# Optimization experiments

Measured on AMD Instinct MI355X. Metric: run time of the kernel, lower is better.

## Reference

```python
import jax, jax.numpy as jnp
import numpy as np

B, C, H, W = 8, 384, 32, 32
NUM_HEADS = 8
HEAD_DIM = C // NUM_HEADS


def setup_inputs() -> dict:
    key = jax.random.key(0)
    k1, k2, k3, k4, k5 = jax.random.split(key, 5)
    s = 1.0 / np.sqrt(C)
    return {
        "x": jax.random.normal(k1, (B, C, H, W), dtype=jnp.float32),
        "w_qkv": jax.random.normal(k2, (3 * C, C), dtype=jnp.float32) * s,   # 1x1 conv == linear over channels
        "b_qkv": jax.random.normal(k3, (3 * C,), dtype=jnp.float32) * 0.01,
        "w_proj": jax.random.normal(k4, (C, C), dtype=jnp.float32) * s,
        "b_proj": jax.random.normal(k5, (C,), dtype=jnp.float32) * 0.01,
    }


def reference(x, w_qkv, b_qkv, w_proj, b_proj):
    b, c, h, w = x.shape
    n = h * w
    scale = HEAD_DIM ** (-0.5)
    # 1x1 conv qkv: (B, 3C, H, W)
    qkv = jnp.einsum('bchw,oc->bohw', x, w_qkv) + b_qkv[None, :, None, None]
    # 'b (three hd d) h0 w0 -> three b hd (h0 w0) d'
    qkv = qkv.reshape(b, 3, NUM_HEADS, HEAD_DIM, n)
    qkv = jnp.transpose(qkv, (1, 0, 2, 4, 3))  # (3, B, heads, N, d)
    q, k, v = qkv[0], qkv[1], qkv[2]
    attn = jnp.einsum('bhnd,bhmd->bhnm', q, k) * scale
    attn = jax.nn.softmax(attn, axis=-1)
    out = jnp.einsum('bhnm,bhmd->bhnd', attn, v)          # (B, heads, N, d)
    out = jnp.transpose(out, (0, 1, 3, 2)).reshape(b, c, h, w)  # b (hd d) h w
    out = jnp.einsum('bchw,oc->bohw', out, w_proj) + b_proj[None, :, None, None]
    return out
```

## Files before the change

kernel.cpp:

```cpp
#include <hip/hip_runtime.h>
#include <hip/hip_bf16.h>

typedef __hip_bfloat16 bf16;
typedef __bf16 bfx8 __attribute__((ext_vector_type(8)));
typedef float f32x4 __attribute__((ext_vector_type(4)));

#define Bk   8
#define Ck   384
#define NHk  8
#define Dk   48
#define Dp   64
#define Nk   1024
#define O3   1152


__device__ __forceinline__ void gload_lds16(const bf16* src, void* dst)
{
    __builtin_amdgcn_global_load_lds(
        (const __attribute__((address_space(1))) void*)src,
        (__attribute__((address_space(3))) void*)dst, 16, 0, 0);
}

__device__ __forceinline__ int pack2(float a, float b)
{
    bf16 ha = __float2bfloat16(a), hb = __float2bfloat16(b);
    unsigned lo = *(unsigned short*)&ha, hi = *(unsigned short*)&hb;
    return (int)(lo | (hi << 16));
}

__device__ __forceinline__ ushort4 pack4(float v0, float v1, float v2, float v3)
{
    bf16 h0 = __float2bfloat16(v0), h1 = __float2bfloat16(v1);
    bf16 h2 = __float2bfloat16(v2), h3 = __float2bfloat16(v3);
    ushort4 pk;
    pk.x = *(unsigned short*)&h0; pk.y = *(unsigned short*)&h1;
    pk.z = *(unsigned short*)&h2; pk.w = *(unsigned short*)&h3;
    return pk;
}

__global__ __launch_bounds__(256) void prep_kernel(
    const float* __restrict__ x, bf16* __restrict__ Xs,
    const float* __restrict__ wq, const float* __restrict__ wp,
    bf16* __restrict__ Wq, bf16* __restrict__ Wp,
    bf16* __restrict__ Qs, bf16* __restrict__ Ks)
{
    const int u = blockIdx.x * 256 + threadIdx.x;
    if (u < 393216) {
        int n = u & 1023, rest = u >> 10;
        int oct = rest % 48, b = rest / 48;
        const float* xb = x + (size_t)b * Ck * Nk;
        float f[8];
        #pragma unroll
        for (int e = 0; e < 8; ++e) f[e] = xb[(size_t)(oct * 8 + e) * Nk + n];
        int4 v = { pack2(f[0], f[1]), pack2(f[2], f[3]),
                   pack2(f[4], f[5]), pack2(f[6], f[7]) };
        bf16* dst = Xs + ((size_t)b * 64 + (n >> 4)) * 6144 + oct * 128 + (n & 15) * 8;
        *(int4*)dst = v;
    } else if (u < 448512) {
        int u1 = u - 393216;
        int o = u1 % 1152, oct = u1 / 1152;
        const float* src = wq + (size_t)o * Ck + oct * 8;
        int4 v = { pack2(src[0], src[1]), pack2(src[2], src[3]),
                   pack2(src[4], src[5]), pack2(src[6], src[7]) };
        bf16* dst = Wq + ((size_t)(o >> 4) * 48 + oct) * 128 + (o & 15) * 8;
        *(int4*)dst = v;
    } else if (u < 466944) {
        int u2 = u - 448512;
        int o = u2 % 384, oct = u2 / 384;
        const float* src = wp + (size_t)o * Ck + oct * 8;
        int4 v = { pack2(src[0], src[1]), pack2(src[2], src[3]),
                   pack2(src[4], src[5]), pack2(src[6], src[7]) };
        bf16* dst = Wp + ((size_t)(o >> 4) * 48 + oct) * 128 + (o & 15) * 8;
        *(int4*)dst = v;
    } else {
        int i = u - 466944;
        int buf = i >> 17;
        int r17 = i & 131071;
        int head = r17 >> 11;
        int r11 = r17 & 2047;
        int g = r11 >> 5, c5 = r11 & 31;
        int cd = 6 + (c5 >> 4), e = c5 & 15;
        bf16* p = (buf ? Ks : Qs) + (size_t)head * 65536 +
                  ((size_t)g * 8 + cd) * 128 + e * 8;
        *(int4*)p = (int4){0, 0, 0, 0};
    }
}

__global__ __launch_bounds__(256) void qkv_mfma_kernel(
    const bf16* __restrict__ Xs, const bf16* __restrict__ Wq,
    const float* __restrict__ bias,
    bf16* __restrict__ Qs, bf16* __restrict__ Ks, bf16* __restrict__ Vs)
{
    __shared__ __align__(16) bf16 Wl[24576];

    const int b    = blockIdx.z;
    const int by   = blockIdx.y;
    const int bx   = blockIdx.x;
    const int o0   = by * 64;
    const int n0   = bx * 128;
    const int wave = threadIdx.x >> 6;
    const int lane = threadIdx.x & 63;
    const int l15  = lane & 15, quad = lane >> 4;
    const int t3   = o0 / Ck;

    {
        const bf16* wsrc = Wq + (size_t)by * 24576;
        #pragma unroll
        for (int i = 0; i < 12; ++i) {
            int f = wave * 12 + i;
            gload_lds16(wsrc + f * 512 + lane * 8, (char*)Wl + f * 1024);
        }
    }

    const bf16* xg[2];
    #pragma unroll
    for (int i = 0; i < 2; ++i)
        xg[i] = Xs + ((size_t)(b * 64 + bx * 8 + wave * 2 + i) * 48) * 128 + lane * 8;
    const bf16* wl = Wl + lane * 8;

    f32x4 acc[8];
    #pragma unroll
    for (int i = 0; i < 8; ++i) acc[i] = (f32x4){0.f, 0.f, 0.f, 0.f};

    asm volatile("s_waitcnt vmcnt(0)" ::: "memory");
    __syncthreads();

    if (t3 < 2) {
        #pragma unroll
        for (int s = 0; s < 12; ++s) {
            bfx8 fx[2], fw[4];
            #pragma unroll
            for (int i = 0; i < 2; ++i) fx[i] = *(const bfx8*)(xg[i] + s * 512);
            #pragma unroll
            for (int j = 0; j < 4; ++j) fw[j] = *(const bfx8*)(wl + j * 6144 + s * 512);
            #pragma unroll
            for (int j = 0; j < 4; ++j)
                #pragma unroll
                for (int i = 0; i < 2; ++i)
                    acc[j * 2 + i] = __builtin_amdgcn_mfma_f32_16x16x32_bf16(
                        fw[j], fx[i], acc[j * 2 + i], 0, 0, 0);
        }
        const float qscale = 0.2082350964f;
        #pragma unroll
        for (int j = 0; j < 4; ++j) {
            int ob = o0 + j * 16 + quad * 4;
            float4 bi = *(const float4*)&bias[ob];
            int r  = ob - t3 * Ck;
            int hd = r / Dk, d0 = r - hd * Dk;
            bf16* hb = (t3 == 0 ? Qs : Ks) + (size_t)(b * NHk + hd) * 65536
                     + (d0 >> 3) * 128 + (d0 & 7);
            #pragma unroll
            for (int i = 0; i < 2; ++i) {
                int npos = n0 + wave * 32 + i * 16 + l15;
                f32x4 a = acc[j * 2 + i];
                float v0 = a[0] + bi.x, v1 = a[1] + bi.y;
                float v2 = a[2] + bi.z, v3 = a[3] + bi.w;
                if (t3 == 0) { v0 *= qscale; v1 *= qscale; v2 *= qscale; v3 *= qscale; }
                *(ushort4*)(hb + (size_t)(npos >> 4) * 1024 + (npos & 15) * 8) =
                    pack4(v0, v1, v2, v3);
            }
        }
    } else {
        #pragma unroll
        for (int s = 0; s < 12; ++s) {
            bfx8 fx[2], fw[4];
            #pragma unroll
            for (int i = 0; i < 2; ++i) fx[i] = *(const bfx8*)(xg[i] + s * 512);
            #pragma unroll
            for (int j = 0; j < 4; ++j) fw[j] = *(const bfx8*)(wl + j * 6144 + s * 512);
            #pragma unroll
            for (int i = 0; i < 2; ++i)
                #pragma unroll
                for (int j = 0; j < 4; ++j)
                    acc[i * 4 + j] = __builtin_amdgcn_mfma_f32_16x16x32_bf16(
                        fx[i], fw[j], acc[i * 4 + j], 0, 0, 0);
        }
        #pragma unroll
        for (int j = 0; j < 4; ++j) {
            int ov = o0 + j * 16 + l15;
            float bi = bias[ov];
            int r  = ov - 2 * Ck;
            int hd = r / Dk, d = r - hd * Dk;
            bf16* vbp = Vs + (size_t)(b * NHk + hd) * 49152
                      + (size_t)(d >> 4) * 16384 + (d & 15) * 8;
            #pragma unroll
            for (int i = 0; i < 2; ++i) {
                int npb = n0 + wave * 32 + i * 16 + quad * 4;
                f32x4 a = acc[i * 4 + j];
                *(ushort4*)(vbp + (size_t)(npb >> 3) * 128 + (npb & 7)) =
                    pack4(a[0] + bi, a[1] + bi, a[2] + bi, a[3] + bi);
            }
        }
    }
}

__global__ __launch_bounds__(256, 2) void attn_kernel(
    const bf16* __restrict__ Qs, const bf16* __restrict__ Ks,
    const bf16* __restrict__ Vs, bf16* __restrict__ AO)
{
    __shared__ __align__(16) bf16 KbL[2][4096];
    __shared__ __align__(16) bf16 VbL[2][3072];
    __shared__ __align__(16) short Ps[4 * 2 * 1152];
    __shared__ float sums[4][2][16];

    const int hd   = blockIdx.x;
    const int b    = blockIdx.y;
    const int bx   = blockIdx.z;
    const int t    = threadIdx.x;
    const int wave = t >> 6;
    const int lane = t & 63;
    const int l15  = lane & 15;
    const int quad = lane >> 4;
    const int grp16 = (bx * 4 + wave) * 2;

    const bf16* qb = Qs + (size_t)(b * NHk + hd) * 65536;
    const bf16* kb = Ks + (size_t)(b * NHk + hd) * 65536;
    const bf16* vb = Vs + (size_t)(b * NHk + hd) * 49152;

    auto stage = [&](int buf, int k0) {
        const bf16* ksrc = kb + (size_t)k0 * 64;
        const bf16* vsrc = vb + (size_t)(k0 >> 3) * 128;
        char* kdst = (char*)&KbL[buf][0];
        char* vdst = (char*)&VbL[buf][0];
        #pragma unroll
        for (int i = 0; i < 4; ++i) {
            const int l = wave + i * 4;
            if (l < 14) {
                const int piece = l >> 1, half = l & 1;
                const bf16* src; char* dst;
                if (piece < 4) {
                    src = ksrc + piece * 1024 + half * 512 + lane * 8;
                    dst = kdst + piece * 2048 + half * 1024;
                } else {
                    const int dc = piece - 4;
                    src = vsrc + (size_t)dc * 16384 + half * 512 + lane * 8;
                    dst = vdst + dc * 2048 + half * 1024;
                }
                gload_lds16(src, dst);
            }
        }
    };

    stage(0, 0);

    bfx8 bq[2][2];
    #pragma unroll
    for (int qt = 0; qt < 2; ++qt) {
        const bf16* qp = qb + ((size_t)(grp16 + qt) * 8 + quad) * 128 + l15 * 8;
        bq[qt][0] = *(const bfx8*)(qp);
        bq[qt][1] = *(const bfx8*)(qp + 512);
    }

    float l_run[2] = {0.f, 0.f};
    f32x4 oacc[2][3];
    #pragma unroll
    for (int qt = 0; qt < 2; ++qt)
        #pragma unroll
        for (int dc = 0; dc < 3; ++dc) oacc[qt][dc] = (f32x4){0.f, 0.f, 0.f, 0.f};

    short* const PsW[2] = { Ps + wave * 2304, Ps + wave * 2304 + 1152 };
    const int lo = quad * 128 + l15 * 8;

    asm volatile("s_waitcnt vmcnt(0)" ::: "memory");
    __syncthreads();

    auto step = [&](int buf, int k0, bool pf) {
        if (pf) stage(buf ^ 1, k0 + 64);

        const bf16* Kc = &KbL[buf][0];
        const bf16* Vc = &VbL[buf][0];

        f32x4 sf[2][4];
        #pragma unroll
        for (int s = 0; s < 4; ++s) {
            const bfx8 kf0 = *(const bfx8*)(Kc + s * 1024 + lo);
            const bfx8 kf1 = *(const bfx8*)(Kc + s * 1024 + 512 + lo);
            #pragma unroll
            for (int qt = 0; qt < 2; ++qt) {
                f32x4 z = (f32x4){0.f, 0.f, 0.f, 0.f};
                z = __builtin_amdgcn_mfma_f32_16x16x32_bf16(kf0, bq[qt][0], z, 0, 0, 0);
                z = __builtin_amdgcn_mfma_f32_16x16x32_bf16(kf1, bq[qt][1], z, 0, 0, 0);
                sf[qt][s] = z;
            }
        }

        #pragma unroll
        for (int qt = 0; qt < 2; ++qt) {
            float lsum = 0.f;
            #pragma unroll
            for (int s = 0; s < 4; ++s) {
                float e0 = __builtin_amdgcn_exp2f(sf[qt][s][0]);
                float e1 = __builtin_amdgcn_exp2f(sf[qt][s][1]);
                float e2 = __builtin_amdgcn_exp2f(sf[qt][s][2]);
                float e3 = __builtin_amdgcn_exp2f(sf[qt][s][3]);
                lsum += (e0 + e1) + (e2 + e3);
                *(ushort4*)&PsW[qt][l15 * 72 + s * 16 + quad * 4] =
                    pack4(e0, e1, e2, e3);
            }
            l_run[qt] += lsum;
        }

        #pragma unroll
        for (int qt = 0; qt < 2; ++qt) {
            const bfx8 ap0 = *(const bfx8*)&PsW[qt][l15 * 72 + quad * 8];
            const bfx8 ap1 = *(const bfx8*)&PsW[qt][l15 * 72 + 32 + quad * 8];
            #pragma unroll
            for (int dc = 0; dc < 3; ++dc) {
                const bfx8 bv0 = *(const bfx8*)(Vc + dc * 1024 + lo);
                const bfx8 bv1 = *(const bfx8*)(Vc + dc * 1024 + 512 + lo);
                oacc[qt][dc] = __builtin_amdgcn_mfma_f32_16x16x32_bf16(
                    ap0, bv0, oacc[qt][dc], 0, 0, 0);
                oacc[qt][dc] = __builtin_amdgcn_mfma_f32_16x16x32_bf16(
                    ap1, bv1, oacc[qt][dc], 0, 0, 0);
            }
        }

        asm volatile("s_waitcnt vmcnt(0)" ::: "memory");
        __syncthreads();
    };

    #pragma unroll 1
    for (int k0 = 0; k0 < Nk; k0 += 128) {
        step(0, k0, true);
        step(1, k0 + 64, k0 + 128 < Nk);
    }

    #pragma unroll
    for (int qt = 0; qt < 2; ++qt) {
        float lt = l_run[qt];
        lt += __shfl_xor(lt, 16, 64);
        lt += __shfl_xor(lt, 32, 64);
        sums[wave][qt][l15] = lt;
    }
    asm volatile("s_waitcnt lgkmcnt(0)" ::: "memory");

    #pragma unroll
    for (int qt = 0; qt < 2; ++qt) {
        short* OsW = PsW[qt];
        #pragma unroll
        for (int r = 0; r < 4; ++r) {
            int qi = quad * 4 + r;
            float rli = 1.0f / sums[wave][qt][qi];
            #pragma unroll
            for (int dcc = 0; dcc < 3; ++dcc) {
                bf16 hb = __float2bfloat16(oacc[qt][dcc][r] * rli);
                OsW[qi * 64 + dcc * 16 + l15] = *(short*)&hb;
            }
        }
    }
    asm volatile("s_waitcnt lgkmcnt(0)" ::: "memory");

    #pragma unroll
    for (int qt = 0; qt < 2; ++qt) {
        bf16* aob = AO + (((size_t)b * 64 + grp16 + qt) * 48 + hd * 6) * 128;
        short* OsW = PsW[qt];
        int u = lane;
        int4 v = *(const int4*)&OsW[(u & 15) * 64 + (u >> 4) * 8];
        *(int4*)(aob + u * 8) = v;
        if (lane < 32) {
            int u2 = 64 + lane;
            int4 v2 = *(const int4*)&OsW[(u2 & 15) * 64 + (u2 >> 4) * 8];
            *(int4*)(aob + u2 * 8) = v2;
        }
    }
}

__global__ __launch_bounds__(256) void proj_mfma_kernel(
    const bf16* __restrict__ AO, const bf16* __restrict__ Wp,
    const float* __restrict__ bias, float* __restrict__ out)
{
    __shared__ __align__(16) bf16 Wl[24576];

    const int b    = blockIdx.z;
    const int by   = blockIdx.y;
    const int bx   = blockIdx.x;
    const int o0   = by * 64;
    const int n0   = bx * 128;
    const int wave = threadIdx.x >> 6;
    const int lane = threadIdx.x & 63;
    const int l15  = lane & 15, quad = lane >> 4;

    {
        const bf16* wsrc = Wp + (size_t)by * 24576;
        #pragma unroll
        for (int i = 0; i < 12; ++i) {
            int f = wave * 12 + i;
            gload_lds16(wsrc + f * 512 + lane * 8, (char*)Wl + f * 1024);
        }
    }

    const bf16* ag[2];
    #pragma unroll
    for (int i = 0; i < 2; ++i)
        ag[i] = AO + ((size_t)(b * 64 + bx * 8 + wave * 2 + i) * 48) * 128 + lane * 8;
    const bf16* wl = Wl + lane * 8;

    f32x4 acc[8];
    #pragma unroll
    for (int i = 0; i < 8; ++i) acc[i] = (f32x4){0.f, 0.f, 0.f, 0.f};

    asm volatile("s_waitcnt vmcnt(0)" ::: "memory");
    __syncthreads();

    #pragma unroll
    for (int s = 0; s < 12; ++s) {
        bfx8 fx[2], fw[4];
        #pragma unroll
        for (int i = 0; i < 2; ++i) fx[i] = *(const bfx8*)(ag[i] + s * 512);
        #pragma unroll
        for (int j = 0; j < 4; ++j) fw[j] = *(const bfx8*)(wl + j * 6144 + s * 512);
        #pragma unroll
        for (int i = 0; i < 2; ++i)
            #pragma unroll
            for (int j = 0; j < 4; ++j)
                acc[i * 4 + j] = __builtin_amdgcn_mfma_f32_16x16x32_bf16(
                    fx[i], fw[j], acc[i * 4 + j], 0, 0, 0);
    }

    #pragma unroll
    for (int j = 0; j < 4; ++j) {
        int o = o0 + j * 16 + l15;
        float bi = bias[o];
        #pragma unroll
        for (int i = 0; i < 2; ++i) {
            int npb = n0 + wave * 32 + i * 16 + quad * 4;
            f32x4 a = acc[i * 4 + j];
            float4 v = { a[0] + bi, a[1] + bi, a[2] + bi, a[3] + bi };
            *(float4*)&out[((size_t)b * Ck + o) * Nk + npb] = v;
        }
    }
}

extern "C" void kernel_launch(void* const* d_in, const int* in_sizes, int n_in,
                              void* d_out, int out_size, void* d_ws, size_t ws_size,
                              hipStream_t stream)
{
    const float* x      = (const float*)d_in[0];
    const float* w_qkv  = (const float*)d_in[1];
    const float* b_qkv  = (const float*)d_in[2];
    const float* w_proj = (const float*)d_in[3];
    const float* b_proj = (const float*)d_in[4];
    float* out = (float*)d_out;

    const size_t XT_SEG = (size_t)Bk * Nk * Ck;
    const size_t WQ_SEG = (size_t)O3 * Ck;
    const size_t WP_SEG = (size_t)Ck * Ck;
    const size_t QK_SEG = (size_t)Bk * NHk * Nk * Dp;
    const size_t V_SEG  = (size_t)Bk * NHk * Dk * Nk;

    bf16* Xs = (bf16*)d_ws;
    bf16* Wq = Xs + XT_SEG;
    bf16* Wp = Wq + WQ_SEG;
    bf16* Qs = Wp + WP_SEG;
    bf16* Ks = Qs + QK_SEG;
    bf16* Vs = Ks + QK_SEG;
    bf16* AO = Vs + V_SEG;

    prep_kernel<<<2848, 256, 0, stream>>>(x, Xs, w_qkv, w_proj, Wq, Wp, Qs, Ks);
    qkv_mfma_kernel<<<dim3(Nk / 128, O3 / 64, Bk), 256, 0, stream>>>(
        Xs, Wq, b_qkv, Qs, Ks, Vs);
    attn_kernel<<<dim3(NHk, Bk, 8), 256, 0, stream>>>(Qs, Ks, Vs, AO);
    proj_mfma_kernel<<<dim3(Nk / 128, Ck / 64, Bk), 256, 0, stream>>>(
        AO, Wp, b_proj, out);
}
```

Measured before the change: 120.1 us.

## Software-pipeline attention: split K/V staging and defer PV by one tile

The attention loop now stages K one tile ahead and V for the current tile separately. The P·V multiply for the previous tile is moved after the current tile's QK/softmax so V loads overlap with compute, using double-buffered P in LDS. The row-sum reduction now uses shuffles instead of an LDS sums array. The QKV and projection GEMMs also issue the first X/AO fragment load before the weight-LDS barrier to hide that latency. The cost is more LDS for P buffers and a longer dependency chain per iteration.

New measurement: 123.4 us. 1.03x slower.

```diff
diff --git a/kernel.cpp b/kernel.cpp
--- a/kernel.cpp
+++ b/kernel.cpp
@@ -118,6 +118,10 @@
         xg[i] = Xs + ((size_t)(b * 64 + bx * 8 + wave * 2 + i) * 48) * 128 + lane * 8;
     const bf16* wl = Wl + lane * 8;
 
+    bfx8 fx0[2];
+    #pragma unroll
+    for (int i = 0; i < 2; ++i) fx0[i] = *(const bfx8*)(xg[i]);
+
     f32x4 acc[8];
     #pragma unroll
     for (int i = 0; i < 8; ++i) acc[i] = (f32x4){0.f, 0.f, 0.f, 0.f};
@@ -130,7 +134,8 @@
         for (int s = 0; s < 12; ++s) {
             bfx8 fx[2], fw[4];
             #pragma unroll
-            for (int i = 0; i < 2; ++i) fx[i] = *(const bfx8*)(xg[i] + s * 512);
+            for (int i = 0; i < 2; ++i)
+                fx[i] = (s == 0) ? fx0[i] : *(const bfx8*)(xg[i] + s * 512);
             #pragma unroll
             for (int j = 0; j < 4; ++j) fw[j] = *(const bfx8*)(wl + j * 6144 + s * 512);
             #pragma unroll
@@ -165,7 +170,8 @@
         for (int s = 0; s < 12; ++s) {
             bfx8 fx[2], fw[4];
             #pragma unroll
-            for (int i = 0; i < 2; ++i) fx[i] = *(const bfx8*)(xg[i] + s * 512);
+            for (int i = 0; i < 2; ++i)
+                fx[i] = (s == 0) ? fx0[i] : *(const bfx8*)(xg[i] + s * 512);
             #pragma unroll
             for (int j = 0; j < 4; ++j) fw[j] = *(const bfx8*)(wl + j * 6144 + s * 512);
             #pragma unroll
@@ -200,8 +206,7 @@
 {
     __shared__ __align__(16) bf16 KbL[2][4096];
     __shared__ __align__(16) bf16 VbL[2][3072];
-    __shared__ __align__(16) short Ps[4 * 2 * 1152];
-    __shared__ float sums[4][2][16];
+    __shared__ __align__(16) short Ps[4 * 4608];
 
     const int hd   = blockIdx.x;
     const int b    = blockIdx.y;
@@ -217,31 +222,30 @@
     const bf16* kb = Ks + (size_t)(b * NHk + hd) * 65536;
     const bf16* vb = Vs + (size_t)(b * NHk + hd) * 49152;
 
-    auto stage = [&](int buf, int k0) {
+    auto stageK = [&](int buf, int k0) {
         const bf16* ksrc = kb + (size_t)k0 * 64;
+        char* kdst = (char*)&KbL[buf][0];
+        #pragma unroll
+        for (int i = 0; i < 2; ++i) {
+            int p = wave + i * 4;
+            gload_lds16(ksrc + p * 512 + lane * 8, kdst + p * 1024);
+        }
+    };
+    auto stageV = [&](int buf, int k0) {
         const bf16* vsrc = vb + (size_t)(k0 >> 3) * 128;
-        char* kdst = (char*)&KbL[buf][0];
         char* vdst = (char*)&VbL[buf][0];
         #pragma unroll
-        for (int i = 0; i < 4; ++i) {
-            const int l = wave + i * 4;
-            if (l < 14) {
-                const int piece = l >> 1, half = l & 1;
-                const bf16* src; char* dst;
-                if (piece < 4) {
-                    src = ksrc + piece * 1024 + half * 512 + lane * 8;
-                    dst = kdst + piece * 2048 + half * 1024;
-                } else {
-                    const int dc = piece - 4;
-                    src = vsrc + (size_t)dc * 16384 + half * 512 + lane * 8;
-                    dst = vdst + dc * 2048 + half * 1024;
-                }
-                gload_lds16(src, dst);
+        for (int i = 0; i < 2; ++i) {
+            int p = wave + i * 4;
+            if (p < 6) {
+                int dc = p >> 1, half = p & 1;
+                gload_lds16(vsrc + (size_t)dc * 16384 + half * 512 + lane * 8,
+                            vdst + dc * 2048 + half * 1024);
             }
         }
     };
 
-    stage(0, 0);
+    stageK(0, 0);
 
     bfx8 bq[2][2];
     #pragma unroll
@@ -258,18 +262,19 @@
         #pragma unroll
         for (int dc = 0; dc < 3; ++dc) oacc[qt][dc] = (f32x4){0.f, 0.f, 0.f, 0.f};
 
-    short* const PsW[2] = { Ps + wave * 2304, Ps + wave * 2304 + 1152 };
+    short* const PsW = Ps + wave * 4608;
     const int lo = quad * 128 + l15 * 8;
 
     asm volatile("s_waitcnt vmcnt(0)" ::: "memory");
     __syncthreads();
 
-    auto step = [&](int buf, int k0, bool pf) {
-        if (pf) stage(buf ^ 1, k0 + 64);
-
-        const bf16* Kc = &KbL[buf][0];
-        const bf16* Vc = &VbL[buf][0];
-
+    #pragma unroll 1
+    for (int c = 0; c < 16; ++c) {
+        const int par = c & 1;
+        if (c < 15) stageK(par ^ 1, (c + 1) * 64);
+        stageV(par, c * 64);
+
+        const bf16* Kc = &KbL[par][0];
         f32x4 sf[2][4];
         #pragma unroll
         for (int s = 0; s < 4; ++s) {
@@ -294,16 +299,43 @@
                 float e2 = __builtin_amdgcn_exp2f(sf[qt][s][2]);
                 float e3 = __builtin_amdgcn_exp2f(sf[qt][s][3]);
                 lsum += (e0 + e1) + (e2 + e3);
-                *(ushort4*)&PsW[qt][l15 * 72 + s * 16 + quad * 4] =
+                *(ushort4*)&PsW[(qt * 2 + par) * 1152 + l15 * 72 + s * 16 + quad * 4] =
                     pack4(e0, e1, e2, e3);
             }
             l_run[qt] += lsum;
         }
 
+        if (c > 0) {
+            const int pp = par ^ 1;
+            const bf16* Vc = &VbL[pp][0];
+            #pragma unroll
+            for (int qt = 0; qt < 2; ++qt) {
+                const short* Pp = &PsW[(qt * 2 + pp) * 1152];
+                const bfx8 ap0 = *(const bfx8*)&Pp[l15 * 72 + quad * 8];
+                const bfx8 ap1 = *(const bfx8*)&Pp[l15 * 72 + 32 + quad * 8];
+                #pragma unroll
+                for (int dc = 0; dc < 3; ++dc) {
+                    const bfx8 bv0 = *(const bfx8*)(Vc + dc * 1024 + lo);
+                    const bfx8 bv1 = *(const bfx8*)(Vc + dc * 1024 + 512 + lo);
+                    oacc[qt][dc] = __builtin_amdgcn_mfma_f32_16x16x32_bf16(
+                        ap0, bv0, oacc[qt][dc], 0, 0, 0);
+                    oacc[qt][dc] = __builtin_amdgcn_mfma_f32_16x16x32_bf16(
+                        ap1, bv1, oacc[qt][dc], 0, 0, 0);
+                }
+            }
+        }
+
+        asm volatile("s_waitcnt vmcnt(0)" ::: "memory");
+        __syncthreads();
+    }
+
+    {
+        const bf16* Vc = &VbL[1][0];
         #pragma unroll
         for (int qt = 0; qt < 2; ++qt) {
-            const bfx8 ap0 = *(const bfx8*)&PsW[qt][l15 * 72 + quad * 8];
-            const bfx8 ap1 = *(const bfx8*)&PsW[qt][l15 * 72 + 32 + quad * 8];
+            const short* Pp = &PsW[(qt * 2 + 1) * 1152];
+            const bfx8 ap0 = *(const bfx8*)&Pp[l15 * 72 + quad * 8];
+            const bfx8 ap1 = *(const bfx8*)&Pp[l15 * 72 + 32 + quad * 8];
             #pragma unroll
             for (int dc = 0; dc < 3; ++dc) {
                 const bfx8 bv0 = *(const bfx8*)(Vc + dc * 1024 + lo);
@@ -314,46 +346,31 @@
                     ap1, bv1, oacc[qt][dc], 0, 0, 0);
             }
         }
-
-        asm volatile("s_waitcnt vmcnt(0)" ::: "memory");
-        __syncthreads();
-    };
-
-    #pragma unroll 1
-    for (int k0 = 0; k0 < Nk; k0 += 128) {
-        step(0, k0, true);
-        step(1, k0 + 64, k0 + 128 < Nk);
-    }
-
+    }
+
+    float ltot[2];
     #pragma unroll
     for (int qt = 0; qt < 2; ++qt) {
         float lt = l_run[qt];
         lt += __shfl_xor(lt, 16, 64);
         lt += __shfl_xor(lt, 32, 64);
-        sums[wave][qt][l15] = lt;
-    }
-    asm volatile("s_waitcnt lgkmcnt(0)" ::: "memory");
+        ltot[qt] = lt;
+    }
 
     #pragma unroll
     for (int qt = 0; qt < 2; ++qt) {
-        short* OsW = PsW[qt];
+        short* OsW = PsW + qt * 2304;
         #pragma unroll
         for (int r = 0; r < 4; ++r) {
             int qi = quad * 4 + r;
-            float rli = 1.0f / sums[wave][qt][qi];
+            float rli = 1.0f / __shfl(ltot[qt], qi, 64);
             #pragma unroll
             for (int dcc = 0; dcc < 3; ++dcc) {
                 bf16 hb = __float2bfloat16(oacc[qt][dcc][r] * rli);
                 OsW[qi * 64 + dcc * 16 + l15] = *(short*)&hb;
             }
         }
-    }
-    asm volatile("s_waitcnt lgkmcnt(0)" ::: "memory");
-
-    #pragma unroll
-    for (int qt = 0; qt < 2; ++qt) {
         bf16* aob = AO + (((size_t)b * 64 + grp16 + qt) * 48 + hd * 6) * 128;
-        short* OsW = PsW[qt];
         int u = lane;
         int4 v = *(const int4*)&OsW[(u & 15) * 64 + (u >> 4) * 8];
         *(int4*)(aob + u * 8) = v;
@@ -395,6 +412,10 @@
         ag[i] = AO + ((size_t)(b * 64 + bx * 8 + wave * 2 + i) * 48) * 128 + lane * 8;
     const bf16* wl = Wl + lane * 8;
 
+    bfx8 fx0[2];
+    #pragma unroll
+    for (int i = 0; i < 2; ++i) fx0[i] = *(const bfx8*)(ag[i]);
+
     f32x4 acc[8];
     #pragma unroll
     for (int i = 0; i < 8; ++i) acc[i] = (f32x4){0.f, 0.f, 0.f, 0.f};
@@ -406,7 +427,8 @@
     for (int s = 0; s < 12; ++s) {
         bfx8 fx[2], fw[4];
         #pragma unroll
-        for (int i = 0; i < 2; ++i) fx[i] = *(const bfx8*)(ag[i] + s * 512);
+        for (int i = 0; i < 2; ++i)
+            fx[i] = (s == 0) ? fx0[i] : *(const bfx8*)(ag[i] + s * 512);
         #pragma unroll
         for (int j = 0; j < 4; ++j) fw[j] = *(const bfx8*)(wl + j * 6144 + s * 512);
         #pragma unroll
```

## Fuse four kernels into one persistent kernel with grid barriers

Applied to the files above, without the earlier changes.

Replaces the prep, QKV GEMM, attention and projection launches with a single persistent kernel of 512 blocks that uses atomic-counter grid barriers between phases. The QKV phase also widens each tile to 256 positions with 16 accumulators per wave, looping over 576 tiles. The goal is to remove per-launch overhead and inter-kernel gaps. In exchange it adds a memset plus spin-wait barriers, relies on all 512 blocks being co-resident (two per CU), and the barrier's timeout break could let phases run early and produce silently wrong results.

Result: slower. 392.4 us (+226.7%).

```diff
diff --git a/kernel.cpp b/kernel.cpp
--- a/kernel.cpp
+++ b/kernel.cpp
@@ -12,6 +12,7 @@
 #define Dp   64
 #define Nk   1024
 #define O3   1152
+#define NBLK 512
 
 
 __device__ __forceinline__ void gload_lds16(const bf16* src, void* dst)
@@ -38,395 +39,401 @@
     return pk;
 }
 
-__global__ __launch_bounds__(256) void prep_kernel(
-    const float* __restrict__ x, bf16* __restrict__ Xs,
-    const float* __restrict__ wq, const float* __restrict__ wp,
-    bf16* __restrict__ Wq, bf16* __restrict__ Wp,
-    bf16* __restrict__ Qs, bf16* __restrict__ Ks)
-{
-    const int u = blockIdx.x * 256 + threadIdx.x;
-    if (u < 393216) {
-        int n = u & 1023, rest = u >> 10;
-        int oct = rest % 48, b = rest / 48;
-        const float* xb = x + (size_t)b * Ck * Nk;
-        float f[8];
-        #pragma unroll
-        for (int e = 0; e < 8; ++e) f[e] = xb[(size_t)(oct * 8 + e) * Nk + n];
-        int4 v = { pack2(f[0], f[1]), pack2(f[2], f[3]),
-                   pack2(f[4], f[5]), pack2(f[6], f[7]) };
-        bf16* dst = Xs + ((size_t)b * 64 + (n >> 4)) * 6144 + oct * 128 + (n & 15) * 8;
-        *(int4*)dst = v;
-    } else if (u < 448512) {
-        int u1 = u - 393216;
-        int o = u1 % 1152, oct = u1 / 1152;
-        const float* src = wq + (size_t)o * Ck + oct * 8;
-        int4 v = { pack2(src[0], src[1]), pack2(src[2], src[3]),
-                   pack2(src[4], src[5]), pack2(src[6], src[7]) };
-        bf16* dst = Wq + ((size_t)(o >> 4) * 48 + oct) * 128 + (o & 15) * 8;
-        *(int4*)dst = v;
-    } else if (u < 466944) {
-        int u2 = u - 448512;
-        int o = u2 % 384, oct = u2 / 384;
-        const float* src = wp + (size_t)o * Ck + oct * 8;
-        int4 v = { pack2(src[0], src[1]), pack2(src[2], src[3]),
-                   pack2(src[4], src[5]), pack2(src[6], src[7]) };
-        bf16* dst = Wp + ((size_t)(o >> 4) * 48 + oct) * 128 + (o & 15) * 8;
-        *(int4*)dst = v;
-    } else {
-        int i = u - 466944;
-        int buf = i >> 17;
-        int r17 = i & 131071;
-        int head = r17 >> 11;
-        int r11 = r17 & 2047;
-        int g = r11 >> 5, c5 = r11 & 31;
-        int cd = 6 + (c5 >> 4), e = c5 & 15;
-        bf16* p = (buf ? Ks : Qs) + (size_t)head * 65536 +
-                  ((size_t)g * 8 + cd) * 128 + e * 8;
-        *(int4*)p = (int4){0, 0, 0, 0};
+__device__ __forceinline__ void grid_barrier(unsigned* cnt)
+{
+    __syncthreads();
+    if (threadIdx.x == 0) {
+        __threadfence();
+        __hip_atomic_fetch_add(cnt, 1u, __ATOMIC_ACQ_REL, __HIP_MEMORY_SCOPE_AGENT);
+        unsigned g = 0;
+        while (__hip_atomic_load(cnt, __ATOMIC_ACQUIRE, __HIP_MEMORY_SCOPE_AGENT)
+                   < (unsigned)NBLK) {
+            __builtin_amdgcn_s_sleep(8);
+            if (++g > 2000000u) break;
+        }
+        __threadfence();
     }
-}
-
-__global__ __launch_bounds__(256) void qkv_mfma_kernel(
-    const bf16* __restrict__ Xs, const bf16* __restrict__ Wq,
-    const float* __restrict__ bias,
-    bf16* __restrict__ Qs, bf16* __restrict__ Ks, bf16* __restrict__ Vs)
-{
-    __shared__ __align__(16) bf16 Wl[24576];
-
-    const int b    = blockIdx.z;
-    const int by   = blockIdx.y;
-    const int bx   = blockIdx.x;
-    const int o0   = by * 64;
-    const int n0   = bx * 128;
-    const int wave = threadIdx.x >> 6;
-    const int lane = threadIdx.x & 63;
+    __syncthreads();
+}
+
+__global__ __launch_bounds__(256, 2) void fused_kernel(
+    const float* __restrict__ x,     const float* __restrict__ wqkv,
+    const float* __restrict__ bqkv,  const float* __restrict__ wproj,
+    const float* __restrict__ bproj, float* __restrict__ out,
+    bf16* __restrict__ Xs, bf16* __restrict__ Wq, bf16* __restrict__ Wp,
+    bf16* __restrict__ Qs, bf16* __restrict__ Ks, bf16* __restrict__ Vs,
+    bf16* __restrict__ AO, unsigned* __restrict__ bars)
+{
+    __shared__ __align__(16) char sh_raw[49152];
+
+    const int bid  = blockIdx.x;
+    const int t    = threadIdx.x;
+    const int wave = t >> 6;
+    const int lane = t & 63;
     const int l15  = lane & 15, quad = lane >> 4;
-    const int t3   = o0 / Ck;
+
+    for (int u = bid * 256 + t; u < 729088; u += 131072) {
+        if (u < 393216) {
+            int n = u & 1023, rest = u >> 10;
+            int oct = rest % 48, b = rest / 48;
+            const float* xb = x + (size_t)b * Ck * Nk;
+            float f[8];
+            #pragma unroll
+            for (int e = 0; e < 8; ++e) f[e] = xb[(size_t)(oct * 8 + e) * Nk + n];
+            int4 v = { pack2(f[0], f[1]), pack2(f[2], f[3]),
+                       pack2(f[4], f[5]), pack2(f[6], f[7]) };
+            bf16* dst = Xs + ((size_t)b * 64 + (n >> 4)) * 6144 + oct * 128 + (n & 15) * 8;
+            *(int4*)dst = v;
+        } else if (u < 448512) {
+            int u1 = u - 393216;
+            int o = u1 % 1152, oct = u1 / 1152;
+            const float* src = wqkv + (size_t)o * Ck + oct * 8;
+            int4 v = { pack2(src[0], src[1]), pack2(src[2], src[3]),
+                       pack2(src[4], src[5]), pack2(src[6], src[7]) };
+            bf16* dst = Wq + ((size_t)(o >> 4) * 48 + oct) * 128 + (o & 15) * 8;
+            *(int4*)dst = v;
+        } else if (u < 466944) {
+            int u2 = u - 448512;
+            int o = u2 % 384, oct = u2 / 384;
+            const float* src = wproj + (size_t)o * Ck + oct * 8;
+            int4 v = { pack2(src[0], src[1]), pack2(src[2], src[3]),
+                       pack2(src[4], src[5]), pack2(src[6], src[7]) };
+            bf16* dst = Wp + ((size_t)(o >> 4) * 48 + oct) * 128 + (o & 15) * 8;
+            *(int4*)dst = v;
+        } else {
+            int i = u - 466944;
+            int buf = i >> 17;
+            int r17 = i & 131071;
+            int head = r17 >> 11;
+            int r11 = r17 & 2047;
+            int g = r11 >> 5, c5 = r11 & 31;
+            int cd = 6 + (c5 >> 4), e = c5 & 15;
+            bf16* p = (buf ? Ks : Qs) + (size_t)head * 65536 +
+                      ((size_t)g * 8 + cd) * 128 + e * 8;
+            *(int4*)p = (int4){0, 0, 0, 0};
+        }
+    }
+
+    grid_barrier(&bars[0]);
+
+    for (int u = bid; u < 576; u += NBLK) {
+        const int bx = u & 3, v_ = u >> 2;
+        const int by = v_ % 18, b = v_ / 18;
+        const int o0 = by * 64, n0 = bx * 256;
+        const int t3 = o0 / Ck;
+        bf16* Wl = (bf16*)sh_raw;
+
+        __syncthreads();
+        {
+            const bf16* wsrc = Wq + (size_t)by * 24576;
+            #pragma unroll
+            for (int i = 0; i < 12; ++i) {
+                int f = wave * 12 + i;
+                gload_lds16(wsrc + f * 512 + lane * 8, sh_raw + f * 1024);
+            }
+        }
+        const bf16* xg[4];
+        #pragma unroll
+        for (int i = 0; i < 4; ++i)
+            xg[i] = Xs + ((size_t)(b * 64 + bx * 16 + wave * 4 + i) * 48) * 128 + lane * 8;
+        const bf16* wl = Wl + lane * 8;
+
+        f32x4 acc[16];
+        #pragma unroll
+        for (int i = 0; i < 16; ++i) acc[i] = (f32x4){0.f, 0.f, 0.f, 0.f};
+
+        asm volatile("s_waitcnt vmcnt(0)" ::: "memory");
+        __syncthreads();
+
+        if (t3 < 2) {
+            #pragma unroll
+            for (int s = 0; s < 12; ++s) {
+                bfx8 fx[4], fw[4];
+                #pragma unroll
+                for (int i = 0; i < 4; ++i) fx[i] = *(const bfx8*)(xg[i] + s * 512);
+                #pragma unroll
+                for (int j = 0; j < 4; ++j) fw[j] = *(const bfx8*)(wl + j * 6144 + s * 512);
+                #pragma unroll
+                for (int j = 0; j < 4; ++j)
+                    #pragma unroll
+                    for (int i = 0; i < 4; ++i)
+                        acc[j * 4 + i] = __builtin_amdgcn_mfma_f32_16x16x32_bf16(
+                            fw[j], fx[i], acc[j * 4 + i], 0, 0, 0);
+            }
+            const float qscale = 0.2082350964f;
+            #pragma unroll
+            for (int j = 0; j < 4; ++j) {
+                int ob = o0 + j * 16 + quad * 4;
+                float4 bi = *(const float4*)&bqkv[ob];
+                int r  = ob - t3 * Ck;
+                int hd = r / Dk, d0 = r - hd * Dk;
+                bf16* hb = (t3 == 0 ? Qs : Ks) + (size_t)(b * NHk + hd) * 65536
+                         + (d0 >> 3) * 128 + (d0 & 7);
+                #pragma unroll
+                for (int i = 0; i < 4; ++i) {
+                    int npos = n0 + wave * 64 + i * 16 + l15;
+                    f32x4 a = acc[j * 4 + i];
+                    float v0 = a[0] + bi.x, v1 = a[1] + bi.y;
+                    float v2 = a[2] + bi.z, v3 = a[3] + bi.w;
+                    if (t3 == 0) { v0 *= qscale; v1 *= qscale; v2 *= qscale; v3 *= qscale; }
+                    *(ushort4*)(hb + (size_t)(npos >> 4) * 1024 + (npos & 15) * 8) =
+                        pack4(v0, v1, v2, v3);
+                }
+            }
+        } else {
+            #pragma unroll
+            for (int s = 0; s < 12; ++s) {
+                bfx8 fx[4], fw[4];
+                #pragma unroll
+                for (int i = 0; i < 4; ++i) fx[i] = *(const bfx8*)(xg[i] + s * 512);
+                #pragma unroll
+                for (int j = 0; j < 4; ++j) fw[j] = *(const bfx8*)(wl + j * 6144 + s * 512);
+                #pragma unroll
+                for (int i = 0; i < 4; ++i)
+                    #pragma unroll
+                    for (int j = 0; j < 4; ++j)
+                        acc[i * 4 + j] = __builtin_amdgcn_mfma_f32_16x16x32_bf16(
+                            fx[i], fw[j], acc[i * 4 + j], 0, 0, 0);
+            }
+            #pragma unroll
+            for (int j = 0; j < 4; ++j) {
+                int ov = o0 + j * 16 + l15;
+                float bi = bqkv[ov];
+                int r  = ov - 2 * Ck;
+                int hd = r / Dk, d = r - hd * Dk;
+                bf16* vbp = Vs + (size_t)(b * NHk + hd) * 49152
+                          + (size_t)(d >> 4) * 16384 + (d & 15) * 8;
+                #pragma unroll
+                for (int i = 0; i < 4; ++i) {
+                    int npb = n0 + wave * 64 + i * 16 + quad * 4;
+                    f32x4 a = acc[i * 4 + j];
+                    *(ushort4*)(vbp + (size_t)(npb >> 3) * 128 + (npb & 7)) =
+                        pack4(a[0] + bi, a[1] + bi, a[2] + bi, a[3] + bi);
+                }
+            }
+        }
+    }
+
+    grid_barrier(&bars[1]);
 
     {
-        const bf16* wsrc = Wq + (size_t)by * 24576;
-        #pragma unroll
-        for (int i = 0; i < 12; ++i) {
-            int f = wave * 12 + i;
-            gload_lds16(wsrc + f * 512 + lane * 8, (char*)Wl + f * 1024);
+        bf16*  KbL  = (bf16*)sh_raw;
+        bf16*  VbL  = (bf16*)(sh_raw + 16384);
+        short* Ps   = (short*)(sh_raw + 28672);
+        float* sums = (float*)(sh_raw + 47104);
+
+        const int hd = bid & 7;
+        const int b  = (bid >> 3) & 7;
+        const int bx = bid >> 6;
+        const int grp16 = (bx * 4 + wave) * 2;
+
+        const bf16* qb = Qs + (size_t)(b * NHk + hd) * 65536;
+        const bf16* kb = Ks + (size_t)(b * NHk + hd) * 65536;
+        const bf16* vb = Vs + (size_t)(b * NHk + hd) * 49152;
+
+        auto stage = [&](int buf, int k0) {
+            const bf16* ksrc = kb + (size_t)k0 * 64;
+            const bf16* vsrc = vb + (size_t)(k0 >> 3) * 128;
+            char* kdst = (char*)(KbL + buf * 4096);
+            char* vdst = (char*)(VbL + buf * 3072);
+            #pragma unroll
+            for (int i = 0; i < 4; ++i) {
+                const int l = wave + i * 4;
+                if (l < 14) {
+                    const int piece = l >> 1, half = l & 1;
+                    const bf16* src; char* dst;
+                    if (piece < 4) {
+                        src = ksrc + piece * 1024 + half * 512 + lane * 8;
+                        dst = kdst + piece * 2048 + half * 1024;
+                    } else {
+                        const int dc = piece - 4;
+                        src = vsrc + (size_t)dc * 16384 + half * 512 + lane * 8;
+                        dst = vdst + dc * 2048 + half * 1024;
+                    }
+                    gload_lds16(src, dst);
+                }
+            }
+        };
+
+        stage(0, 0);
+
+        bfx8 bq[2][2];
+        #pragma unroll
+        for (int qt = 0; qt < 2; ++qt) {
+            const bf16* qp = qb + ((size_t)(grp16 + qt) * 8 + quad) * 128 + l15 * 8;
+            bq[qt][0] = *(const bfx8*)(qp);
+            bq[qt][1] = *(const bfx8*)(qp + 512);
+        }
+
+        float l_run[2] = {0.f, 0.f};
+        f32x4 oacc[2][3];
+        #pragma unroll
+        for (int qt = 0; qt < 2; ++qt)
+            #pragma unroll
+            for (int dc = 0; dc < 3; ++dc) oacc[qt][dc] = (f32x4){0.f, 0.f, 0.f, 0.f};
+
+        short* const PsW[2] = { Ps + wave * 2304, Ps + wave * 2304 + 1152 };
+        const int lo = quad * 128 + l15 * 8;
+
+        asm volatile("s_waitcnt vmcnt(0)" ::: "memory");
+        __syncthreads();
+
+        auto step = [&](int buf, int k0, bool pf) {
+            if (pf) stage(buf ^ 1, k0 + 64);
+
+            const bf16* Kc = KbL + buf * 4096;
+            const bf16* Vc = VbL + buf * 3072;
+
+            f32x4 sf[2][4];
+            #pragma unroll
+            for (int s = 0; s < 4; ++s) {
+                const bfx8 kf0 = *(const bfx8*)(Kc + s * 1024 + lo);
+                const bfx8 kf1 = *(const bfx8*)(Kc + s * 1024 + 512 + lo);
+                #pragma unroll
+                for (int qt = 0; qt < 2; ++qt) {
+                    f32x4 z = (f32x4){0.f, 0.f, 0.f, 0.f};
+                    z = __builtin_amdgcn_mfma_f32_16x16x32_bf16(kf0, bq[qt][0], z, 0, 0, 0);
+                    z = __builtin_amdgcn_mfma_f32_16x16x32_bf16(kf1, bq[qt][1], z, 0, 0, 0);
+                    sf[qt][s] = z;
+                }
+            }
+
+            #pragma unroll
+            for (int qt = 0; qt < 2; ++qt) {
+                float lsum = 0.f;
+                #pragma unroll
+                for (int s = 0; s < 4; ++s) {
+                    float e0 = __builtin_amdgcn_exp2f(sf[qt][s][0]);
+                    float e1 = __builtin_amdgcn_exp2f(sf[qt][s][1]);
+                    float e2 = __builtin_amdgcn_exp2f(sf[qt][s][2]);
+                    float e3 = __builtin_amdgcn_exp2f(sf[qt][s][3]);
+                    lsum += (e0 + e1) + (e2 + e3);
+                    *(ushort4*)&PsW[qt][l15 * 72 + s * 16 + quad * 4] =
+                        pack4(e0, e1, e2, e3);
+                }
+                l_run[qt] += lsum;
+            }
+
+            #pragma unroll
+            for (int qt = 0; qt < 2; ++qt) {
+                const bfx8 ap0 = *(const bfx8*)&PsW[qt][l15 * 72 + quad * 8];
+                const bfx8 ap1 = *(const bfx8*)&PsW[qt][l15 * 72 + 32 + quad * 8];
+                #pragma unroll
+                for (int dc = 0; dc < 3; ++dc) {
+                    const bfx8 bv0 = *(const bfx8*)(Vc + dc * 1024 + lo);
+                    const bfx8 bv1 = *(const bfx8*)(Vc + dc * 1024 + 512 + lo);
+                    oacc[qt][dc] = __builtin_amdgcn_mfma_f32_16x16x32_bf16(
+                        ap0, bv0, oacc[qt][dc], 0, 0, 0);
+                    oacc[qt][dc] = __builtin_amdgcn_mfma_f32_16x16x32_bf16(
+                        ap1, bv1, oacc[qt][dc], 0, 0, 0);
+                }
+            }
+
+            asm volatile("s_waitcnt vmcnt(0)" ::: "memory");
+            __syncthreads();
+        };
+
+        #pragma unroll 1
+        for (int k0 = 0; k0 < Nk; k0 += 128) {
+            step(0, k0, true);
+            step(1, k0 + 64, k0 + 128 < Nk);
+        }
+
+        #pragma unroll
+        for (int qt = 0; qt < 2; ++qt) {
+            float lt = l_run[qt];
+            lt += __shfl_xor(lt, 16, 64);
+            lt += __shfl_xor(lt, 32, 64);
+            sums[(wave * 2 + qt) * 16 + l15] = lt;
+        }
+        asm volatile("s_waitcnt lgkmcnt(0)" ::: "memory");
+
+        #pragma unroll
+        for (int qt = 0; qt < 2; ++qt) {
+            short* OsW = PsW[qt];
+            #pragma unroll
+            for (int r = 0; r < 4; ++r) {
+                int qi = quad * 4 + r;
+                float rli = 1.0f / sums[(wave * 2 + qt) * 16 + qi];
+                #pragma unroll
+                for (int dcc = 0; dcc < 3; ++dcc) {
+                    bf16 hb = __float2bfloat16(oacc[qt][dcc][r] * rli);
+                    OsW[qi * 64 + dcc * 16 + l15] = *(short*)&hb;
+                }
+            }
+        }
+        asm volatile("s_waitcnt lgkmcnt(0)" ::: "memory");
+
+        #pragma unroll
+        for (int qt = 0; qt < 2; ++qt) {
+            bf16* aob = AO + (((size_t)b * 64 + grp16 + qt) * 48 + hd * 6) * 128;
+            short* OsW = PsW[qt];
+            int u = lane;
+            int4 v = *(const int4*)&OsW[(u & 15) * 64 + (u >> 4) * 8];
+            *(int4*)(aob + u * 8) = v;
+            if (lane < 32) {
+                int u2 = 64 + lane;
+                int4 v2 = *(const int4*)&OsW[(u2 & 15) * 64 + (u2 >> 4) * 8];
+                *(int4*)(aob + u2 * 8) = v2;
+            }
         }
     }
 
-    const bf16* xg[2];
-    #pragma unroll
-    for (int i = 0; i < 2; ++i)
-        xg[i] = Xs + ((size_t)(b * 64 + bx * 8 + wave * 2 + i) * 48) * 128 + lane * 8;
-    const bf16* wl = Wl + lane * 8;
-
-    f32x4 acc[8];
-    #pragma unroll
-    for (int i = 0; i < 8; ++i) acc[i] = (f32x4){0.f, 0.f, 0.f, 0.f};
-
-    asm volatile("s_waitcnt vmcnt(0)" ::: "memory");
-    __syncthreads();
-
-    if (t3 < 2) {
+    grid_barrier(&bars[2]);
+
+    if (bid < 192) {
+        const int b = bid / 24, r_ = bid % 24;
+        const int by = r_ >> 2, bx = r_ & 3;
+        const int o0 = by * 64, n0 = bx * 256;
+        bf16* Wl = (bf16*)sh_raw;
+
+        {
+            const bf16* wsrc = Wp + (size_t)by * 24576;
+            #pragma unroll
+            for (int i = 0; i < 12; ++i) {
+                int f = wave * 12 + i;
+                gload_lds16(wsrc + f * 512 + lane * 8, sh_raw + f * 1024);
+            }
+        }
+        const bf16* ag[4];
+        #pragma unroll
+        for (int i = 0; i < 4; ++i)
+            ag[i] = AO + ((size_t)(b * 64 + bx * 16 + wave * 4 + i) * 48) * 128 + lane * 8;
+        const bf16* wl = Wl + lane * 8;
+
+        f32x4 acc[16];
+        #pragma unroll
+        for (int i = 0; i < 16; ++i) acc[i] = (f32x4){0.f, 0.f, 0.f, 0.f};
+
+        asm volatile("s_waitcnt vmcnt(0)" ::: "memory");
+        __syncthreads();
+
         #pragma unroll
         for (int s = 0; s < 12; ++s) {
-            bfx8 fx[2], fw[4];
-            #pragma unroll
-            for (int i = 0; i < 2; ++i) fx[i] = *(const bfx8*)(xg[i] + s * 512);
+            bfx8 fx[4], fw[4];
+            #pragma unroll
+            for (int i = 0; i < 4; ++i) fx[i] = *(const bfx8*)(ag[i] + s * 512);
             #pragma unroll
             for (int j = 0; j < 4; ++j) fw[j] = *(const bfx8*)(wl + j * 6144 + s * 512);
             #pragma unroll
-            for (int j = 0; j < 4; ++j)
-                #pragma unroll
-                for (int i = 0; i < 2; ++i)
-                    acc[j * 2 + i] = __builtin_amdgcn_mfma_f32_16x16x32_bf16(
-                        fw[j], fx[i], acc[j * 2 + i], 0, 0, 0);
-        }
-        const float qscale = 0.2082350964f;
-        #pragma unroll
-        for (int j = 0; j < 4; ++j) {
-            int ob = o0 + j * 16 + quad * 4;
-            float4 bi = *(const float4*)&bias[ob];
-            int r  = ob - t3 * Ck;
-            int hd = r / Dk, d0 = r - hd * Dk;
-            bf16* hb = (t3 == 0 ? Qs : Ks) + (size_t)(b * NHk + hd) * 65536
-                     + (d0 >> 3) * 128 + (d0 & 7);
-            #pragma unroll
-            for (int i = 0; i < 2; ++i) {
-                int npos = n0 + wave * 32 + i * 16 + l15;
-                f32x4 a = acc[j * 2 + i];
-                float v0 = a[0] + bi.x, v1 = a[1] + bi.y;
-                float v2 = a[2] + bi.z, v3 = a[3] + bi.w;
-                if (t3 == 0) { v0 *= qscale; v1 *= qscale; v2 *= qscale; v3 *= qscale; }
-                *(ushort4*)(hb + (size_t)(npos >> 4) * 1024 + (npos & 15) * 8) =
-                    pack4(v0, v1, v2, v3);
-            }
-        }
-    } else {
-        #pragma unroll
-        for (int s = 0; s < 12; ++s) {
-            bfx8 fx[2], fw[4];
-            #pragma unroll
-            for (int i = 0; i < 2; ++i) fx[i] = *(const bfx8*)(xg[i] + s * 512);
-            #pragma unroll
-            for (int j = 0; j < 4; ++j) fw[j] = *(const bfx8*)(wl + j * 6144 + s * 512);
-            #pragma unroll
-            for (int i = 0; i < 2; ++i)
+            for (int i = 0; i < 4; ++i)
                 #pragma unroll
                 for (int j = 0; j < 4; ++j)
                     acc[i * 4 + j] = __builtin_amdgcn_mfma_f32_16x16x32_bf16(
                         fx[i], fw[j], acc[i * 4 + j], 0, 0, 0);
         }
+
         #pragma unroll
         for (int j = 0; j < 4; ++j) {
-            int ov = o0 + j * 16 + l15;
-            float bi = bias[ov];
-            int r  = ov - 2 * Ck;
-            int hd = r / Dk, d = r - hd * Dk;
-            bf16* vbp = Vs + (size_t)(b * NHk + hd) * 49152
-                      + (size_t)(d >> 4) * 16384 + (d & 15) * 8;
-            #pragma unroll
-            for (int i = 0; i < 2; ++i) {
-                int npb = n0 + wave * 32 + i * 16 + quad * 4;
+            int o = o0 + j * 16 + l15;
+            float bi = bproj[o];
+            #pragma unroll
+            for (int i = 0; i < 4; ++i) {
+                int npb = n0 + wave * 64 + i * 16 + quad * 4;
                 f32x4 a = acc[i * 4 + j];
-                *(ushort4*)(vbp + (size_t)(npb >> 3) * 128 + (npb & 7)) =
-                    pack4(a[0] + bi, a[1] + bi, a[2] + bi, a[3] + bi);
-            }
-        }
-    }
-}
-
-__global__ __launch_bounds__(256, 2) void attn_kernel(
-    const bf16* __restrict__ Qs, const bf16* __restrict__ Ks,
-    const bf16* __restrict__ Vs, bf16* __restrict__ AO)
-{
-    __shared__ __align__(16) bf16 KbL[2][4096];
-    __shared__ __align__(16) bf16 VbL[2][3072];
-    __shared__ __align__(16) short Ps[4 * 2 * 1152];
-    __shared__ float sums[4][2][16];
-
-    const int hd   = blockIdx.x;
-    const int b    = blockIdx.y;
-    const int bx   = blockIdx.z;
-    const int t    = threadIdx.x;
-    const int wave = t >> 6;
-    const int lane = t & 63;
-    const int l15  = lane & 15;
-    const int quad = lane >> 4;
-    const int grp16 = (bx * 4 + wave) * 2;
-
-    const bf16* qb = Qs + (size_t)(b * NHk + hd) * 65536;
-    const bf16* kb = Ks + (size_t)(b * NHk + hd) * 65536;
-    const bf16* vb = Vs + (size_t)(b * NHk + hd) * 49152;
-
-    auto stage = [&](int buf, int k0) {
-        const bf16* ksrc = kb + (size_t)k0 * 64;
-        const bf16* vsrc = vb + (size_t)(k0 >> 3) * 128;
-        char* kdst = (char*)&KbL[buf][0];
-        char* vdst = (char*)&VbL[buf][0];
-        #pragma unroll
-        for (int i = 0; i < 4; ++i) {
-            const int l = wave + i * 4;
-            if (l < 14) {
-                const int piece = l >> 1, half = l & 1;
-                const bf16* src; char* dst;
-                if (piece < 4) {
-                    src = ksrc + piece * 1024 + half * 512 + lane * 8;
-                    dst = kdst + piece * 2048 + half * 1024;
-                } else {
-                    const int dc = piece - 4;
-                    src = vsrc + (size_t)dc * 16384 + half * 512 + lane * 8;
-                    dst = vdst + dc * 2048 + half * 1024;
-                }
-                gload_lds16(src, dst);
-            }
-        }
-    };
-
-    stage(0, 0);
-
-    bfx8 bq[2][2];
-    #pragma unroll
-    for (int qt = 0; qt < 2; ++qt) {
-        const bf16* qp = qb + ((size_t)(grp16 + qt) * 8 + quad) * 128 + l15 * 8;
-        bq[qt][0] = *(const bfx8*)(qp);
-        bq[qt][1] = *(const bfx8*)(qp + 512);
-    }
-
-    float l_run[2] = {0.f, 0.f};
-    f32x4 oacc[2][3];
-    #pragma unroll
-    for (int qt = 0; qt < 2; ++qt)
-        #pragma unroll
-        for (int dc = 0; dc < 3; ++dc) oacc[qt][dc] = (f32x4){0.f, 0.f, 0.f, 0.f};
-
-    short* const PsW[2] = { Ps + wave * 2304, Ps + wave * 2304 + 1152 };
-    const int lo = quad * 128 + l15 * 8;
-
-    asm volatile("s_waitcnt vmcnt(0)" ::: "memory");
-    __syncthreads();
-
-    auto step = [&](int buf, int k0, bool pf) {
-        if (pf) stage(buf ^ 1, k0 + 64);
-
-        const bf16* Kc = &KbL[buf][0];
-        const bf16* Vc = &VbL[buf][0];
-
-        f32x4 sf[2][4];
-        #pragma unroll
-        for (int s = 0; s < 4; ++s) {
-            const bfx8 kf0 = *(const bfx8*)(Kc + s * 1024 + lo);
-            const bfx8 kf1 = *(const bfx8*)(Kc + s * 1024 + 512 + lo);
-            #pragma unroll
-            for (int qt = 0; qt < 2; ++qt) {
-                f32x4 z = (f32x4){0.f, 0.f, 0.f, 0.f};
-                z = __builtin_amdgcn_mfma_f32_16x16x32_bf16(kf0, bq[qt][0], z, 0, 0, 0);
-                z = __builtin_amdgcn_mfma_f32_16x16x32_bf16(kf1, bq[qt][1], z, 0, 0, 0);
-                sf[qt][s] = z;
-            }
-        }
-
-        #pragma unroll
-        for (int qt = 0; qt < 2; ++qt) {
-            float lsum = 0.f;
-            #pragma unroll
-            for (int s = 0; s < 4; ++s) {
-                float e0 = __builtin_amdgcn_exp2f(sf[qt][s][0]);
-                float e1 = __builtin_amdgcn_exp2f(sf[qt][s][1]);
-                float e2 = __builtin_amdgcn_exp2f(sf[qt][s][2]);
-                float e3 = __builtin_amdgcn_exp2f(sf[qt][s][3]);
-                lsum += (e0 + e1) + (e2 + e3);
-                *(ushort4*)&PsW[qt][l15 * 72 + s * 16 + quad * 4] =
-                    pack4(e0, e1, e2, e3);
-            }
-            l_run[qt] += lsum;
-        }
-
-        #pragma unroll
-        for (int qt = 0; qt < 2; ++qt) {
-            const bfx8 ap0 = *(const bfx8*)&PsW[qt][l15 * 72 + quad * 8];
-            const bfx8 ap1 = *(const bfx8*)&PsW[qt][l15 * 72 + 32 + quad * 8];
-            #pragma unroll
-            for (int dc = 0; dc < 3; ++dc) {
-                const bfx8 bv0 = *(const bfx8*)(Vc + dc * 1024 + lo);
-                const bfx8 bv1 = *(const bfx8*)(Vc + dc * 1024 + 512 + lo);
-                oacc[qt][dc] = __builtin_amdgcn_mfma_f32_16x16x32_bf16(
-                    ap0, bv0, oacc[qt][dc], 0, 0, 0);
-                oacc[qt][dc] = __builtin_amdgcn_mfma_f32_16x16x32_bf16(
-                    ap1, bv1, oacc[qt][dc], 0, 0, 0);
-            }
-        }
-
-        asm volatile("s_waitcnt vmcnt(0)" ::: "memory");
-        __syncthreads();
-    };
-
-    #pragma unroll 1
-    for (int k0 = 0; k0 < Nk; k0 += 128) {
-        step(0, k0, true);
-        step(1, k0 + 64, k0 + 128 < Nk);
-    }
-
-    #pragma unroll
-    for (int qt = 0; qt < 2; ++qt) {
-        float lt = l_run[qt];
-        lt += __shfl_xor(lt, 16, 64);
-        lt += __shfl_xor(lt, 32, 64);
-        sums[wave][qt][l15] = lt;
-    }
-    asm volatile("s_waitcnt lgkmcnt(0)" ::: "memory");
-
-    #pragma unroll
-    for (int qt = 0; qt < 2; ++qt) {
-        short* OsW = PsW[qt];
-        #pragma unroll
-        for (int r = 0; r < 4; ++r) {
-            int qi = quad * 4 + r;
-            float rli = 1.0f / sums[wave][qt][qi];
-            #pragma unroll
-            for (int dcc = 0; dcc < 3; ++dcc) {
-                bf16 hb = __float2bfloat16(oacc[qt][dcc][r] * rli);
-                OsW[qi * 64 + dcc * 16 + l15] = *(short*)&hb;
-            }
-        }
-    }
-    asm volatile("s_waitcnt lgkmcnt(0)" ::: "memory");
-
-    #pragma unroll
-    for (int qt = 0; qt < 2; ++qt) {
-        bf16* aob = AO + (((size_t)b * 64 + grp16 + qt) * 48 + hd * 6) * 128;
-        short* OsW = PsW[qt];
-        int u = lane;
-        int4 v = *(const int4*)&OsW[(u & 15) * 64 + (u >> 4) * 8];
-        *(int4*)(aob + u * 8) = v;
-        if (lane < 32) {
-            int u2 = 64 + lane;
-            int4 v2 = *(const int4*)&OsW[(u2 & 15) * 64 + (u2 >> 4) * 8];
-            *(int4*)(aob + u2 * 8) = v2;
-        }
-    }
-}
-
-__global__ __launch_bounds__(256) void proj_mfma_kernel(
-    const bf16* __restrict__ AO, const bf16* __restrict__ Wp,
-    const float* __restrict__ bias, float* __restrict__ out)
-{
-    __shared__ __align__(16) bf16 Wl[24576];
-
-    const int b    = blockIdx.z;
-    const int by   = blockIdx.y;
-    const int bx   = blockIdx.x;
-    const int o0   = by * 64;
-    const int n0   = bx * 128;
-    const int wave = threadIdx.x >> 6;
-    const int lane = threadIdx.x & 63;
-    const int l15  = lane & 15, quad = lane >> 4;
-
-    {
-        const bf16* wsrc = Wp + (size_t)by * 24576;
-        #pragma unroll
-        for (int i = 0; i < 12; ++i) {
-            int f = wave * 12 + i;
-            gload_lds16(wsrc + f * 512 + lane * 8, (char*)Wl + f * 1024);
-        }
-    }
-
-    const bf16* ag[2];
-    #pragma unroll
-    for (int i = 0; i < 2; ++i)
-        ag[i] = AO + ((size_t)(b * 64 + bx * 8 + wave * 2 + i) * 48) * 128 + lane * 8;
-    const bf16* wl = Wl + lane * 8;
-
-    f32x4 acc[8];
-    #pragma unroll
-    for (int i = 0; i < 8; ++i) acc[i] = (f32x4){0.f, 0.f, 0.f, 0.f};
-
-    asm volatile("s_waitcnt vmcnt(0)" ::: "memory");
-    __syncthreads();
-
-    #pragma unroll
-    for (int s = 0; s < 12; ++s) {
-        bfx8 fx[2], fw[4];
-        #pragma unroll
-        for (int i = 0; i < 2; ++i) fx[i] = *(const bfx8*)(ag[i] + s * 512);
-        #pragma unroll
-        for (int j = 0; j < 4; ++j) fw[j] = *(const bfx8*)(wl + j * 6144 + s * 512);
-        #pragma unroll
-        for (int i = 0; i < 2; ++i)
-            #pragma unroll
-            for (int j = 0; j < 4; ++j)
-                acc[i * 4 + j] = __builtin_amdgcn_mfma_f32_16x16x32_bf16(
-                    fx[i], fw[j], acc[i * 4 + j], 0, 0, 0);
-    }
-
-    #pragma unroll
-    for (int j = 0; j < 4; ++j) {
-        int o = o0 + j * 16 + l15;
-        float bi = bias[o];
-        #pragma unroll
-        for (int i = 0; i < 2; ++i) {
-            int npb = n0 + wave * 32 + i * 16 + quad * 4;
-            f32x4 a = acc[i * 4 + j];
-            float4 v = { a[0] + bi, a[1] + bi, a[2] + bi, a[3] + bi };
-            *(float4*)&out[((size_t)b * Ck + o) * Nk + npb] = v;
+                float4 v = { a[0] + bi, a[1] + bi, a[2] + bi, a[3] + bi };
+                *(float4*)&out[((size_t)b * Ck + o) * Nk + npb] = v;
+            }
         }
     }
 }
@@ -447,6 +454,7 @@
     const size_t WP_SEG = (size_t)Ck * Ck;
     const size_t QK_SEG = (size_t)Bk * NHk * Nk * Dp;
     const size_t V_SEG  = (size_t)Bk * NHk * Dk * Nk;
+    const size_t AO_SEG = (size_t)Bk * Nk * Ck;
 
     bf16* Xs = (bf16*)d_ws;
     bf16* Wq = Xs + XT_SEG;
@@ -455,11 +463,10 @@
     bf16* Ks = Qs + QK_SEG;
     bf16* Vs = Ks + QK_SEG;
     bf16* AO = Vs + V_SEG;
-
-    prep_kernel<<<2848, 256, 0, stream>>>(x, Xs, w_qkv, w_proj, Wq, Wp, Qs, Ks);
-    qkv_mfma_kernel<<<dim3(Nk / 128, O3 / 64, Bk), 256, 0, stream>>>(
-        Xs, Wq, b_qkv, Qs, Ks, Vs);
-    attn_kernel<<<dim3(NHk, Bk, 8), 256, 0, stream>>>(Qs, Ks, Vs, AO);
-    proj_mfma_kernel<<<dim3(Nk / 128, Ck / 64, Bk), 256, 0, stream>>>(
-        AO, Wp, b_proj, out);
-}
+    unsigned* bars = (unsigned*)(AO + AO_SEG);
+
+    hipMemsetAsync(bars, 0, 64, stream);
+    fused_kernel<<<NBLK, 256, 0, stream>>>(
+        x, w_qkv, b_qkv, w_proj, b_proj, out,
+        Xs, Wq, Wp, Qs, Ks, Vs, AO, bars);
+}
```
